# Performance work log

Hardware: AMD Instinct MI355X
Metric: run time of the kernel (lower is better)

Reference implementation:

```python
import jax, jax.numpy as jnp
import numpy as np

DIM = 64  # per-head dim used for the sqrt scale


def setup_inputs() -> dict:
    key = jax.random.key(0)
    kq, kk, kv, ke, kf = jax.random.split(key, 5)
    B, N, d, k = 32, 4096, 64, 256
    Q = jax.random.normal(kq, (B, N, d), dtype=jnp.float32)
    K = jax.random.normal(kk, (B, N, d), dtype=jnp.float32)
    V = jax.random.normal(kv, (B, N, d), dtype=jnp.float32)
    E = jax.random.normal(ke, (N, k), dtype=jnp.float32) * (1.0 / np.sqrt(N))
    F = jax.random.normal(kf, (N, k), dtype=jnp.float32) * (1.0 / np.sqrt(N))
    return {"Q": Q, "K": K, "V": V, "E": E, "F": F}


def reference(Q, K, V, E, F):
    # Linformer head: K^T E -> [B,d,k]; Q (K^T E) / sqrt(d) -> [B,N,k]
    K_proj = jnp.einsum('bnd,nk->bdk', K, E)          # low-rank key projection
    scores = jnp.einsum('bnd,bdk->bnk', Q, K_proj) / jnp.sqrt(jnp.float32(DIM))
    P_bar = jax.nn.softmax(scores, axis=2)            # [B,N,k]
    # (V^T F)^T -> [B,k,d]
    V_proj = jnp.einsum('bnd,nk->bkd', V, F)
    return jnp.einsum('bnk,bkd->bnd', P_bar, V_proj)  # [B,N,d]
```

## Files before the change

kernel.cpp:

```cpp
#include <hip/hip_runtime.h>
#include <hip/hip_bf16.h>

#define BB 32
#define NN 4096
#define DDIM 64
#define NCH 8

typedef __attribute__((ext_vector_type(8)))  short bf16x8;
typedef __attribute__((ext_vector_type(16))) float f32x16;
typedef __attribute__((ext_vector_type(4)))  float f32x4;

static __device__ inline unsigned pk(float a, float b) {
  union { __hip_bfloat162 h; unsigned u; } c;
  c.h = __float22bfloat162_rn(float2{a, b});
  return c.u;
}

static __device__ inline bf16x8 pack8(const float* f) {
  union { unsigned u[4]; bf16x8 v; } r;
  r.u[0] = pk(f[0], f[1]); r.u[1] = pk(f[2], f[3]);
  r.u[2] = pk(f[4], f[5]); r.u[3] = pk(f[6], f[7]);
  return r.v;
}

template <int MAT>
static __device__ inline void proj_core6(
    const float* __restrict__ Gbig,
    const float* __restrict__ Gsml,
    float* __restrict__ Cg,
    unsigned short (*lds)[10240], int chunk)
{
  const int t = threadIdx.x;
  const int w = t >> 6, l = t & 63, h = l >> 5, lr = l & 31;
  const int hs = t >> 8;
  const int colB = t & 255;
  const int gS = (t >> 6) & 3;
  const int colS = t & 63;

  const int n00 = chunk * 512;

  f32x16 acc[2];
#pragma unroll
  for (int j = 0; j < 2; ++j)
#pragma unroll
    for (int q = 0; q < 16; ++q) acc[j][q] = 0.f;

  float xb[16], xs[8], yb[16], ys[8];

  auto loadset = [&](float (&vb)[16], float (&vs)[8], int step) {
    const float* qb = Gbig + (long)(n00 + step * 32 + hs * 16) * 256 + colB;
#pragma unroll
    for (int i = 0; i < 16; ++i) vb[i] = qb[(long)i * 256];
    if (t < 256) {
      const float* qs = Gsml + (long)(n00 + step * 32 + gS * 8) * 64 + colS;
#pragma unroll
      for (int j = 0; j < 8; ++j) vs[j] = qs[(long)j * 64];
    }
  };

  auto writeset = [&](int buf, float (&vb)[16], float (&vs)[8]) {
#pragma unroll
    for (int gg = 0; gg < 2; ++gg) {
      const int g = hs * 2 + gg;
      *(bf16x8*)&lds[buf][(g * 256 + colB) * 8] = pack8(&vb[gg * 8]);
    }
    if (t < 256)
      *(bf16x8*)&lds[buf][8192 + (gS * 64 + colS) * 8] = pack8(vs);
  };

  auto consume = [&](int buf) {
#pragma unroll
    for (int s2 = 0; s2 < 2; ++s2) {
      const int g = s2 * 2 + h;
      bf16x8 Bg = *(const bf16x8*)&lds[buf][(g * 256 + w * 32 + lr) * 8];
      bf16x8 S0 = *(const bf16x8*)&lds[buf][8192 + (g * 64 + lr) * 8];
      bf16x8 S1 = *(const bf16x8*)&lds[buf][8192 + (g * 64 + 32 + lr) * 8];
      if (MAT == 0) {
        acc[0] = __builtin_amdgcn_mfma_f32_32x32x16_bf16(Bg, S0, acc[0], 0, 0, 0);
        acc[1] = __builtin_amdgcn_mfma_f32_32x32x16_bf16(Bg, S1, acc[1], 0, 0, 0);
      } else {
        acc[0] = __builtin_amdgcn_mfma_f32_32x32x16_bf16(S0, Bg, acc[0], 0, 0, 0);
        acc[1] = __builtin_amdgcn_mfma_f32_32x32x16_bf16(S1, Bg, acc[1], 0, 0, 0);
      }
    }
  };

  loadset(xb, xs, 0);
  loadset(yb, ys, 1);

#pragma unroll 1
  for (int tt = 0; tt < 16; tt += 2) {
    writeset(0, xb, xs);
    if (tt + 2 < 16) loadset(xb, xs, tt + 2);
    __syncthreads();
    consume(0);
    writeset(1, yb, ys);
    if (tt + 3 < 16) loadset(yb, ys, tt + 3);
    __syncthreads();
    consume(1);
  }

#pragma unroll
  for (int j = 0; j < 2; ++j)
#pragma unroll
    for (int i = 0; i < 16; ++i) {
      const int ro = (i & 3) + 8 * (i >> 2) + 4 * h;
      if (MAT == 0) {
        const int row = w * 32 + ro;
        const int col = j * 32 + lr;
        Cg[row * 64 + col] = acc[j][i];
      } else {
        const int row = j * 32 + ro;
        const int col = w * 32 + lr;
        Cg[row * 256 + col] = acc[j][i];
      }
    }
}

__global__ __launch_bounds__(512, 4) void proj_gemm(
    const float* __restrict__ Kg, const float* __restrict__ Vg,
    const float* __restrict__ Eg, const float* __restrict__ Fg,
    float* __restrict__ KpP, float* __restrict__ VpP)
{
  __shared__ unsigned short lds[2][10240];

  const int blk = blockIdx.x;
  const int chunk = blk % NCH;
  const int mat = (blk / NCH) & 1, b = blk / (2 * NCH);
  const long PSTR = (long)BB * 16384;

  if (mat == 0) {
    proj_core6<0>(Eg, Kg + (long)b * NN * DDIM,
                  KpP + (long)chunk * PSTR + b * 16384, lds, chunk);
  } else {
    proj_core6<1>(Fg, Vg + (long)b * NN * DDIM,
                  VpP + (long)chunk * PSTR + b * 16384, lds, chunk);
  }
}

__global__ __launch_bounds__(256) void reduce_cvt(
    const float* __restrict__ KpP, const float* __restrict__ VpP,
    unsigned short* __restrict__ Kpb, unsigned short* __restrict__ Vpb)
{
  const int blk = blockIdx.x;
  const float* src = (blk < 512) ? KpP : VpP;
  unsigned short* dst = (blk < 512) ? Kpb : Vpb;
  const long i = (long)(blk & 511) * 1024 + threadIdx.x * 4;
  float a0 = 0.f, a1 = 0.f, a2 = 0.f, a3 = 0.f;
#pragma unroll
  for (int cch = 0; cch < NCH; ++cch) {
    const float4 p = *(const float4*)(src + (long)cch * (BB * 16384) + i);
    a0 += p.x; a1 += p.y; a2 += p.z; a3 += p.w;
  }
  uint2 o;
  o.x = pk(a0, a1); o.y = pk(a2, a3);
  *(uint2*)(dst + i) = o;
}

__global__ __launch_bounds__(256, 4) void attn2_kernel(
    const float* __restrict__ Qg, const unsigned short* __restrict__ Kpb,
    const unsigned short* __restrict__ Vpb, float* __restrict__ Og)
{
  __shared__ char smem[32768];

  const int blk = blockIdx.x;
  const int b = blk >> 5, rg = blk & 31;
  const int t = threadIdx.x, w = t >> 6, l = t & 63;
  const int h = l >> 5, lr = l & 31;
  const int row0 = rg * 128 + w * 32;

  const unsigned short* Kp = Kpb + (long)b * 16384;
  const unsigned short* Vp = Vpb + (long)b * 16384;

  bf16x8 Bq[4];
#pragma unroll
  for (int kk = 0; kk < 4; ++kk) {
    const float* qp = Qg + ((long)b * NN + row0 + lr) * 64 + kk * 16 + h * 8;
    float4 x = *(const float4*)qp;
    float4 y = *(const float4*)(qp + 4);
    union { unsigned u[4]; bf16x8 v; } r;
    r.u[0] = pk(x.x, x.y); r.u[1] = pk(x.z, x.w);
    r.u[2] = pk(y.x, y.y); r.u[3] = pk(y.z, y.w);
    Bq[kk] = r.v;
  }

  {
    const uint4* gk = (const uint4*)Kp;
#pragma unroll
    for (int i = 0; i < 8; ++i) {
      int u = i * 256 + t;
      uint4 x = gk[u];
      int kbyte = (u * 16) ^ (((u >> 3) & 7) << 4);
      *(uint4*)(smem + kbyte) = x;
    }
  }
  __syncthreads();

  f32x16 o[2];
#pragma unroll
  for (int dt = 0; dt < 2; ++dt)
#pragma unroll
    for (int q = 0; q < 16; ++q) o[dt][q] = 0.f;
  float rowpart = 0.f;

  union UV { uint4 u; bf16x8 v; };
  const int swz = (lr & 7) << 4;

#pragma unroll
  for (int kt = 0; kt < 8; ++kt) {
    bf16x8 Av[2][2];
#pragma unroll
    for (int dt = 0; dt < 2; ++dt)
#pragma unroll
      for (int kc = 0; kc < 2; ++kc)
        Av[dt][kc] = *(const bf16x8*)(Vp + (long)(dt * 32 + lr) * 256 + (kt * 2 + kc) * 16 + h * 8);

    bf16x8 Ak[4];
#pragma unroll
    for (int kk = 0; kk < 4; ++kk) {
      int byte = ((kt * 32 + lr) * 128 + kk * 32 + h * 16) ^ swz;
      Ak[kk] = *(const bf16x8*)(smem + byte);
    }

    f32x16 s;
#pragma unroll
    for (int q = 0; q < 16; ++q) s[q] = 0.f;
#pragma unroll
    for (int kk = 0; kk < 4; ++kk)
      s = __builtin_amdgcn_mfma_f32_32x32x16_bf16(Ak[kk], Bq[kk], s, 0, 0, 0);

    float p[16];
#pragma unroll
    for (int q = 0; q < 16; ++q) p[q] = exp2f(s[q] * 0.1803368801f);
    rowpart += (((p[0] + p[1]) + (p[2] + p[3])) + ((p[4] + p[5]) + (p[6] + p[7])))
             + (((p[8] + p[9]) + (p[10] + p[11])) + ((p[12] + p[13]) + (p[14] + p[15])));

    unsigned wv[8];
#pragma unroll
    for (int m = 0; m < 8; ++m) wv[m] = pk(p[2 * m], p[2 * m + 1]);
    unsigned r02 = __shfl_xor(h ? wv[0] : wv[2], 32);
    unsigned r13 = __shfl_xor(h ? wv[1] : wv[3], 32);
    unsigned r46 = __shfl_xor(h ? wv[4] : wv[6], 32);
    unsigned r57 = __shfl_xor(h ? wv[5] : wv[7], 32);
    UV c0, c1;
    if (h == 0) {
      c0.u = uint4{wv[0], wv[1], r02, r13};
      c1.u = uint4{wv[4], wv[5], r46, r57};
    } else {
      c0.u = uint4{r02, r13, wv[2], wv[3]};
      c1.u = uint4{r46, r57, wv[6], wv[7]};
    }
    o[0] = __builtin_amdgcn_mfma_f32_32x32x16_bf16(Av[0][0], c0.v, o[0], 0, 0, 0);
    o[0] = __builtin_amdgcn_mfma_f32_32x32x16_bf16(Av[0][1], c1.v, o[0], 0, 0, 0);
    o[1] = __builtin_amdgcn_mfma_f32_32x32x16_bf16(Av[1][0], c0.v, o[1], 0, 0, 0);
    o[1] = __builtin_amdgcn_mfma_f32_32x32x16_bf16(Av[1][1], c1.v, o[1], 0, 0, 0);
  }

  __syncthreads();
  float* O_lds = (float*)smem;

  {
    float rowsum = rowpart + __shfl_xor(rowpart, 32);
    float inv = __builtin_amdgcn_rcpf(rowsum);
    const int r = w * 32 + lr;
#pragma unroll
    for (int dt = 0; dt < 2; ++dt)
#pragma unroll
      for (int qg = 0; qg < 4; ++qg) {
        f32x4 vq;
        vq[0] = o[dt][qg * 4 + 0] * inv;
        vq[1] = o[dt][qg * 4 + 1] * inv;
        vq[2] = o[dt][qg * 4 + 2] * inv;
        vq[3] = o[dt][qg * 4 + 3] * inv;
        int cd = dt * 8 + 2 * qg + h;
        int cp = cd ^ (r & 15);
        *(f32x4*)&O_lds[r * 64 + cp * 4] = vq;
      }
  }
  __syncthreads();

  const long obase = ((long)b * NN + rg * 128) * 64;
#pragma unroll
  for (int i = 0; i < 8; ++i) {
    int ci = i * 256 + t;
    int rr = ci >> 4, cc = ci & 15, cp = cc ^ (rr & 15);
    *(float4*)(Og + obase + rr * 64 + cc * 4) = *(const float4*)&O_lds[rr * 64 + cp * 4];
  }
}

extern "C" void kernel_launch(void* const* d_in, const int* in_sizes, int n_in,
                              void* d_out, int out_size, void* d_ws, size_t ws_size,
                              hipStream_t stream) {
  const float* Q = (const float*)d_in[0];
  const float* K = (const float*)d_in[1];
  const float* V = (const float*)d_in[2];
  const float* E = (const float*)d_in[3];
  const float* F = (const float*)d_in[4];
  float* out = (float*)d_out;

  char* ws = (char*)d_ws;
  float*          KpP = (float*)(ws);
  float*          VpP = (float*)(ws + (16l << 20));
  unsigned short* Kpb = (unsigned short*)(ws + (32l << 20));
  unsigned short* Vpb = (unsigned short*)(ws + (33l << 20));

  proj_gemm<<<dim3(512), dim3(512), 0, stream>>>(K, V, E, F, KpP, VpP);

  reduce_cvt<<<dim3(1024), dim3(256), 0, stream>>>(KpP, VpP, Kpb, Vpb);

  attn2_kernel<<<dim3(1024), dim3(256), 0, stream>>>(Q, Kpb, Vpb, out);
}
```

Before: 197.9 us.

## Process two row tiles per wave and double-buffer K/V fragment loads

The attention kernel now handles 256 rows per block, two 32-row tiles per wave, so each K and V fragment loaded feeds twice as many MFMAs. K fragments are read straight from global memory instead of being staged in LDS, and loads for the next key tile are issued ahead of the current tile's compute, separated by sched_barriers. The grid is halved, the output staging buffer becomes 64 KB of dynamic shared memory, and launch bounds drop to 2 blocks per SU. This raises register pressure and lowers occupancy, and it also switches to the raw exp2 builtin.

```diff
diff --git a/kernel.cpp b/kernel.cpp
--- a/kernel.cpp
+++ b/kernel.cpp
@@ -157,121 +157,123 @@
   *(uint2*)(dst + i) = o;
 }
 
-__global__ __launch_bounds__(256, 4) void attn2_kernel(
+__global__ __launch_bounds__(256, 2) void attn2_kernel(
     const float* __restrict__ Qg, const unsigned short* __restrict__ Kpb,
     const unsigned short* __restrict__ Vpb, float* __restrict__ Og)
 {
-  __shared__ char smem[32768];
+  extern __shared__ float O_lds[];
 
   const int blk = blockIdx.x;
-  const int b = blk >> 5, rg = blk & 31;
+  const int b = blk >> 4, rg = blk & 15;
   const int t = threadIdx.x, w = t >> 6, l = t & 63;
   const int h = l >> 5, lr = l & 31;
-  const int row0 = rg * 128 + w * 32;
+  const int rbase = rg * 256 + w * 64;
 
   const unsigned short* Kp = Kpb + (long)b * 16384;
   const unsigned short* Vp = Vpb + (long)b * 16384;
 
-  bf16x8 Bq[4];
-#pragma unroll
-  for (int kk = 0; kk < 4; ++kk) {
-    const float* qp = Qg + ((long)b * NN + row0 + lr) * 64 + kk * 16 + h * 8;
-    float4 x = *(const float4*)qp;
-    float4 y = *(const float4*)(qp + 4);
-    union { unsigned u[4]; bf16x8 v; } r;
-    r.u[0] = pk(x.x, x.y); r.u[1] = pk(x.z, x.w);
-    r.u[2] = pk(y.x, y.y); r.u[3] = pk(y.z, y.w);
-    Bq[kk] = r.v;
-  }
-
-  {
-    const uint4* gk = (const uint4*)Kp;
-#pragma unroll
-    for (int i = 0; i < 8; ++i) {
-      int u = i * 256 + t;
-      uint4 x = gk[u];
-      int kbyte = (u * 16) ^ (((u >> 3) & 7) << 4);
-      *(uint4*)(smem + kbyte) = x;
-    }
-  }
-  __syncthreads();
-
-  f32x16 o[2];
-#pragma unroll
-  for (int dt = 0; dt < 2; ++dt)
-#pragma unroll
-    for (int q = 0; q < 16; ++q) o[dt][q] = 0.f;
-  float rowpart = 0.f;
+  bf16x8 Bq[2][4];
+#pragma unroll
+  for (int rt = 0; rt < 2; ++rt)
+#pragma unroll
+    for (int kk = 0; kk < 4; ++kk) {
+      const float* qp = Qg + ((long)b * NN + rbase + rt * 32 + lr) * 64 + kk * 16 + h * 8;
+      float4 x = *(const float4*)qp;
+      float4 y = *(const float4*)(qp + 4);
+      union { unsigned u[4]; bf16x8 v; } r;
+      r.u[0] = pk(x.x, x.y); r.u[1] = pk(x.z, x.w);
+      r.u[2] = pk(y.x, y.y); r.u[3] = pk(y.z, y.w);
+      Bq[rt][kk] = r.v;
+    }
+
+  f32x16 o[2][2];
+#pragma unroll
+  for (int rt = 0; rt < 2; ++rt)
+#pragma unroll
+    for (int dt = 0; dt < 2; ++dt)
+#pragma unroll
+      for (int q = 0; q < 16; ++q) o[rt][dt][q] = 0.f;
+  float rowpart[2] = {0.f, 0.f};
 
   union UV { uint4 u; bf16x8 v; };
-  const int swz = (lr & 7) << 4;
-
-#pragma unroll
-  for (int kt = 0; kt < 8; ++kt) {
-    bf16x8 Av[2][2];
+
+  auto LDK = [&](int kt, bf16x8 (&Ak)[4], bf16x8 (&Av)[4]) {
+#pragma unroll
+    for (int kk = 0; kk < 4; ++kk)
+      Ak[kk] = *(const bf16x8*)(Kp + (long)(kt * 32 + lr) * 64 + kk * 16 + h * 8);
 #pragma unroll
     for (int dt = 0; dt < 2; ++dt)
 #pragma unroll
       for (int kc = 0; kc < 2; ++kc)
-        Av[dt][kc] = *(const bf16x8*)(Vp + (long)(dt * 32 + lr) * 256 + (kt * 2 + kc) * 16 + h * 8);
-
-    bf16x8 Ak[4];
-#pragma unroll
-    for (int kk = 0; kk < 4; ++kk) {
-      int byte = ((kt * 32 + lr) * 128 + kk * 32 + h * 16) ^ swz;
-      Ak[kk] = *(const bf16x8*)(smem + byte);
-    }
-
-    f32x16 s;
-#pragma unroll
-    for (int q = 0; q < 16; ++q) s[q] = 0.f;
-#pragma unroll
-    for (int kk = 0; kk < 4; ++kk)
-      s = __builtin_amdgcn_mfma_f32_32x32x16_bf16(Ak[kk], Bq[kk], s, 0, 0, 0);
-
-    float p[16];
-#pragma unroll
-    for (int q = 0; q < 16; ++q) p[q] = exp2f(s[q] * 0.1803368801f);
-    rowpart += (((p[0] + p[1]) + (p[2] + p[3])) + ((p[4] + p[5]) + (p[6] + p[7])))
-             + (((p[8] + p[9]) + (p[10] + p[11])) + ((p[12] + p[13]) + (p[14] + p[15])));
-
-    unsigned wv[8];
-#pragma unroll
-    for (int m = 0; m < 8; ++m) wv[m] = pk(p[2 * m], p[2 * m + 1]);
-    unsigned r02 = __shfl_xor(h ? wv[0] : wv[2], 32);
-    unsigned r13 = __shfl_xor(h ? wv[1] : wv[3], 32);
-    unsigned r46 = __shfl_xor(h ? wv[4] : wv[6], 32);
-    unsigned r57 = __shfl_xor(h ? wv[5] : wv[7], 32);
-    UV c0, c1;
-    if (h == 0) {
-      c0.u = uint4{wv[0], wv[1], r02, r13};
-      c1.u = uint4{wv[4], wv[5], r46, r57};
-    } else {
-      c0.u = uint4{r02, r13, wv[2], wv[3]};
-      c1.u = uint4{r46, r57, wv[6], wv[7]};
-    }
-    o[0] = __builtin_amdgcn_mfma_f32_32x32x16_bf16(Av[0][0], c0.v, o[0], 0, 0, 0);
-    o[0] = __builtin_amdgcn_mfma_f32_32x32x16_bf16(Av[0][1], c1.v, o[0], 0, 0, 0);
-    o[1] = __builtin_amdgcn_mfma_f32_32x32x16_bf16(Av[1][0], c0.v, o[1], 0, 0, 0);
-    o[1] = __builtin_amdgcn_mfma_f32_32x32x16_bf16(Av[1][1], c1.v, o[1], 0, 0, 0);
-  }
-
-  __syncthreads();
-  float* O_lds = (float*)smem;
-
-  {
-    float rowsum = rowpart + __shfl_xor(rowpart, 32);
+        Av[dt * 2 + kc] = *(const bf16x8*)(Vp + (long)(dt * 32 + lr) * 256 + (kt * 2 + kc) * 16 + h * 8);
+  };
+
+  auto UNIT = [&](bf16x8 (&Ak)[4], bf16x8 (&Av)[4]) {
+#pragma unroll
+    for (int rt = 0; rt < 2; ++rt) {
+      f32x16 s;
+#pragma unroll
+      for (int q = 0; q < 16; ++q) s[q] = 0.f;
+#pragma unroll
+      for (int kk = 0; kk < 4; ++kk)
+        s = __builtin_amdgcn_mfma_f32_32x32x16_bf16(Ak[kk], Bq[rt][kk], s, 0, 0, 0);
+
+      float p[16];
+#pragma unroll
+      for (int q = 0; q < 16; ++q)
+        p[q] = __builtin_amdgcn_exp2f(s[q] * 0.1803368801f);
+      rowpart[rt] += (((p[0] + p[1]) + (p[2] + p[3])) + ((p[4] + p[5]) + (p[6] + p[7])))
+                   + (((p[8] + p[9]) + (p[10] + p[11])) + ((p[12] + p[13]) + (p[14] + p[15])));
+
+      unsigned wv[8];
+#pragma unroll
+      for (int m = 0; m < 8; ++m) wv[m] = pk(p[2 * m], p[2 * m + 1]);
+      unsigned r02 = __shfl_xor(h ? wv[0] : wv[2], 32);
+      unsigned r13 = __shfl_xor(h ? wv[1] : wv[3], 32);
+      unsigned r46 = __shfl_xor(h ? wv[4] : wv[6], 32);
+      unsigned r57 = __shfl_xor(h ? wv[5] : wv[7], 32);
+      UV c0, c1;
+      if (h == 0) {
+        c0.u = uint4{wv[0], wv[1], r02, r13};
+        c1.u = uint4{wv[4], wv[5], r46, r57};
+      } else {
+        c0.u = uint4{r02, r13, wv[2], wv[3]};
+        c1.u = uint4{r46, r57, wv[6], wv[7]};
+      }
+      o[rt][0] = __builtin_amdgcn_mfma_f32_32x32x16_bf16(Av[0], c0.v, o[rt][0], 0, 0, 0);
+      o[rt][0] = __builtin_amdgcn_mfma_f32_32x32x16_bf16(Av[1], c1.v, o[rt][0], 0, 0, 0);
+      o[rt][1] = __builtin_amdgcn_mfma_f32_32x32x16_bf16(Av[2], c0.v, o[rt][1], 0, 0, 0);
+      o[rt][1] = __builtin_amdgcn_mfma_f32_32x32x16_bf16(Av[3], c1.v, o[rt][1], 0, 0, 0);
+    }
+  };
+
+  bf16x8 AkA[4], AvA[4], AkB[4], AvB[4];
+  LDK(0, AkA, AvA);
+
+#pragma unroll
+  for (int kt = 0; kt < 8; kt += 2) {
+    if (kt + 1 < 8) LDK(kt + 1, AkB, AvB);
+    __builtin_amdgcn_sched_barrier(0);
+    UNIT(AkA, AvA);
+    if (kt + 2 < 8) LDK(kt + 2, AkA, AvA);
+    __builtin_amdgcn_sched_barrier(0);
+    UNIT(AkB, AvB);
+  }
+
+#pragma unroll
+  for (int rt = 0; rt < 2; ++rt) {
+    float rowsum = rowpart[rt] + __shfl_xor(rowpart[rt], 32);
     float inv = __builtin_amdgcn_rcpf(rowsum);
-    const int r = w * 32 + lr;
+    const int r = w * 64 + rt * 32 + lr;
 #pragma unroll
     for (int dt = 0; dt < 2; ++dt)
 #pragma unroll
       for (int qg = 0; qg < 4; ++qg) {
         f32x4 vq;
-        vq[0] = o[dt][qg * 4 + 0] * inv;
-        vq[1] = o[dt][qg * 4 + 1] * inv;
-        vq[2] = o[dt][qg * 4 + 2] * inv;
-        vq[3] = o[dt][qg * 4 + 3] * inv;
+        vq[0] = o[rt][dt][qg * 4 + 0] * inv;
+        vq[1] = o[rt][dt][qg * 4 + 1] * inv;
+        vq[2] = o[rt][dt][qg * 4 + 2] * inv;
+        vq[3] = o[rt][dt][qg * 4 + 3] * inv;
         int cd = dt * 8 + 2 * qg + h;
         int cp = cd ^ (r & 15);
         *(f32x4*)&O_lds[r * 64 + cp * 4] = vq;
@@ -279,9 +281,9 @@
   }
   __syncthreads();
 
-  const long obase = ((long)b * NN + rg * 128) * 64;
-#pragma unroll
-  for (int i = 0; i < 8; ++i) {
+  const long obase = ((long)b * NN + rg * 256) * 64;
+#pragma unroll
+  for (int i = 0; i < 16; ++i) {
     int ci = i * 256 + t;
     int rr = ci >> 4, cc = ci & 15, cp = cc ^ (rr & 15);
     *(float4*)(Og + obase + rr * 64 + cc * 4) = *(const float4*)&O_lds[rr * 64 + cp * 4];
@@ -304,9 +306,12 @@
   unsigned short* Kpb = (unsigned short*)(ws + (32l << 20));
   unsigned short* Vpb = (unsigned short*)(ws + (33l << 20));
 
+  hipFuncSetAttribute((const void*)attn2_kernel,
+                      hipFuncAttributeMaxDynamicSharedMemorySize, 65536);
+
   proj_gemm<<<dim3(512), dim3(512), 0, stream>>>(K, V, E, F, KpP, VpP);
 
   reduce_cvt<<<dim3(1024), dim3(256), 0, stream>>>(KpP, VpP, Kpb, Vpb);
 
-  attn2_kernel<<<dim3(1024), dim3(256), 0, stream>>>(Q, Kpb, Vpb, out);
-}
+  attn2_kernel<<<dim3(512), dim3(256), 65536, stream>>>(Q, Kpb, Vpb, out);
+}
```

Result: slower. 244.9 us (+23.7%).
